# Kernel optimization log

Measured on AMD Instinct MI355X. Metric: run time of the kernel, lower is better.

The kernel has to match this reference:

```python
import jax, jax.numpy as jnp
import numpy as np

B, L, H, K = 4, 4096, 2048, 4
EPS = 1e-5

def setup_inputs() -> dict:
    key = jax.random.key(0)
    k1, k2, k3, k4 = jax.random.split(key, 4)
    x = jax.random.normal(k1, (B, L, H), dtype=jnp.float32)
    # depthwise Conv1d weight: (out_channels=H, in_channels/groups=1, K)
    w = jax.random.normal(k2, (H, 1, K), dtype=jnp.float32) * (1.0 / np.sqrt(K))
    gamma = jax.random.uniform(k3, (H,), dtype=jnp.float32, minval=0.5, maxval=1.5)
    beta = jax.random.normal(k4, (H,), dtype=jnp.float32) * 0.05
    return {"x": x, "w": w, "gamma": gamma, "beta": beta}

def reference(x, w, gamma, beta):
    # x: (B, L, H) -> (B, H, L) channels-first like torch Conv1d
    xc = jnp.transpose(x, (0, 2, 1))
    k = w.shape[-1]
    h = w.shape[0]
    # causal depthwise conv: left-pad K-1, groups = H
    y = jax.lax.conv_general_dilated(
        xc, w,
        window_strides=(1,),
        padding=[(k - 1, 0)],
        feature_group_count=h,
        dimension_numbers=("NCH", "OIH", "NCH"),
    )
    # residual: x_padded[:, :, K-1:] == original xc
    y = y + xc
    y = jnp.transpose(y, (0, 2, 1))  # (B, L, H)
    # LayerNorm over hidden dim
    mu = jnp.mean(y, axis=-1, keepdims=True)
    var = jnp.mean(jnp.square(y - mu), axis=-1, keepdims=True)
    out = (y - mu) * jax.lax.rsqrt(var + EPS) * gamma + beta
    return out
```

## Files before the change

kernel.cpp:

```cpp
#include <hip/hip_runtime.h>

constexpr int B = 4;
constexpr int L = 4096;
constexpr int H = 2048;
constexpr int KTAP = 4;
constexpr float EPS = 1e-5f;

constexpr int THREADS = 256;
constexpr int H4 = H / 4;
constexpr int COLS = H4 / THREADS;
constexpr int ROWS = 8;
constexpr int TILES = (B * L) / ROWS;
constexpr int TPB = L / ROWS;
constexpr int NXCD = 8;
constexpr int WAVES = THREADS / 64;

__global__ __launch_bounds__(THREADS)
void fused_conv_res_ln(const float4* __restrict__ x4,
                       const float4* __restrict__ w4,
                       const float4* __restrict__ g4,
                       const float4* __restrict__ bt4,
                       float4* __restrict__ o4)
{
    const int bid     = blockIdx.x;
    const int logical = (bid & (NXCD - 1)) * (TILES / NXCD) + (bid >> 3);
    const int b       = logical / TPB;
    const int tile    = logical - b * TPB;
    const int l0      = tile * ROWS;
    const int t       = threadIdx.x;

    const size_t rowbase = (size_t)b * L;

    float4 xw[COLS][KTAP];
    float4 wc[COLS][4];
    float4 gg[COLS], bb[COLS];
    int    jj[COLS];

    #pragma unroll
    for (int c = 0; c < COLS; ++c) {
        const int j = t + c * THREADS;
        jj[c] = j;
        #pragma unroll
        for (int k = 0; k < 4; ++k) wc[c][k] = w4[4 * j + k];
        gg[c] = g4[j];
        bb[c] = bt4[j];
        #pragma unroll
        for (int k = 0; k < 3; ++k) {
            const int lr = l0 - 3 + k;
            xw[c][k] = (lr >= 0) ? x4[(rowbase + lr) * H4 + j]
                                 : make_float4(0.f, 0.f, 0.f, 0.f);
        }
        xw[c][3] = x4[(rowbase + l0) * H4 + j];
    }

    __shared__ float s_sum[ROWS][WAVES];
    __shared__ float s_sq [ROWS][WAVES];
    const int wave = t >> 6;
    const int lane = t & 63;

    #pragma unroll
    for (int r = 0; r < ROWS; ++r) {
        float4 xn[COLS];
        if (r + 1 < ROWS) {
            #pragma unroll
            for (int c = 0; c < COLS; ++c)
                xn[c] = x4[(rowbase + l0 + r + 1) * H4 + jj[c]];
        }

        float y[COLS][4];
        float sum = 0.f, sq = 0.f;
        #pragma unroll
        for (int c = 0; c < COLS; ++c) {
            const float4 a0 = xw[c][0], a1 = xw[c][1], a2 = xw[c][2], a3 = xw[c][3];
            y[c][0] = a0.x * wc[c][0].x + a1.x * wc[c][0].y + a2.x * wc[c][0].z + a3.x * wc[c][0].w + a3.x;
            y[c][1] = a0.y * wc[c][1].x + a1.y * wc[c][1].y + a2.y * wc[c][1].z + a3.y * wc[c][1].w + a3.y;
            y[c][2] = a0.z * wc[c][2].x + a1.z * wc[c][2].y + a2.z * wc[c][2].z + a3.z * wc[c][2].w + a3.z;
            y[c][3] = a0.w * wc[c][3].x + a1.w * wc[c][3].y + a2.w * wc[c][3].z + a3.w * wc[c][3].w + a3.w;
            sum += y[c][0] + y[c][1] + y[c][2] + y[c][3];
            sq  += y[c][0] * y[c][0] + y[c][1] * y[c][1]
                 + y[c][2] * y[c][2] + y[c][3] * y[c][3];
        }

        #pragma unroll
        for (int off = 32; off > 0; off >>= 1) {
            sum += __shfl_down(sum, off, 64);
            sq  += __shfl_down(sq,  off, 64);
        }
        if (lane == 0) { s_sum[r][wave] = sum; s_sq[r][wave] = sq; }
        __syncthreads();

        float tot = 0.f, totq = 0.f;
        #pragma unroll
        for (int i = 0; i < WAVES; ++i) { tot += s_sum[r][i]; totq += s_sq[r][i]; }

        const float inv_h = 1.0f / (float)H;
        const float mu    = tot * inv_h;
        const float var   = totq * inv_h - mu * mu;
        const float rstd  = rsqrtf(var + EPS);

        #pragma unroll
        for (int c = 0; c < COLS; ++c) {
            float4 o;
            o.x = (y[c][0] - mu) * rstd * gg[c].x + bb[c].x;
            o.y = (y[c][1] - mu) * rstd * gg[c].y + bb[c].y;
            o.z = (y[c][2] - mu) * rstd * gg[c].z + bb[c].z;
            o.w = (y[c][3] - mu) * rstd * gg[c].w + bb[c].w;
            o4[(rowbase + l0 + r) * H4 + jj[c]] = o;
        }

        #pragma unroll
        for (int c = 0; c < COLS; ++c) {
            xw[c][0] = xw[c][1];
            xw[c][1] = xw[c][2];
            xw[c][2] = xw[c][3];
            if (r + 1 < ROWS) xw[c][3] = xn[c];
        }
    }
}

extern "C" void kernel_launch(void* const* d_in, const int* in_sizes, int n_in,
                              void* d_out, int out_size, void* d_ws, size_t ws_size,
                              hipStream_t stream) {
    const float4* x     = (const float4*)d_in[0];
    const float4* w     = (const float4*)d_in[1];
    const float4* gamma = (const float4*)d_in[2];
    const float4* beta  = (const float4*)d_in[3];
    float4* out = (float4*)d_out;

    dim3 grid(TILES);
    dim3 block(THREADS);
    fused_conv_res_ln<<<grid, block, 0, stream>>>(x, w, gamma, beta, out);
}
```

Baseline: 249.0 us.

## Map one wave per row and drop block-level LayerNorm reduction

Restructures the kernel so each 64-lane wave handles a whole hidden row (8 float4 per lane) instead of a 256-thread block sweeping an 8-row tile with a sliding register window. The row statistics now come from a wave-only xor-shuffle reduction, which removes the shared-memory stage and the per-row __syncthreads. The cost is that each row now re-reads its three predecessor rows from global memory (4x logical x reads, expected to hit cache) and reloads weights, gamma and beta per row. Launch bounds now request 4 blocks per CU to raise occupancy.

```diff
diff --git a/kernel.cpp b/kernel.cpp
--- a/kernel.cpp
+++ b/kernel.cpp
@@ -3,19 +3,17 @@
 constexpr int B = 4;
 constexpr int L = 4096;
 constexpr int H = 2048;
-constexpr int KTAP = 4;
 constexpr float EPS = 1e-5f;
 
+constexpr int H4 = H / 4;
 constexpr int THREADS = 256;
-constexpr int H4 = H / 4;
-constexpr int COLS = H4 / THREADS;
-constexpr int ROWS = 8;
-constexpr int TILES = (B * L) / ROWS;
-constexpr int TPB = L / ROWS;
+constexpr int WPB = THREADS / 64;
+constexpr int NROWS = B * L;
+constexpr int GRID = NROWS / WPB;
 constexpr int NXCD = 8;
-constexpr int WAVES = THREADS / 64;
+constexpr int CHUNK = GRID / NXCD;
 
-__global__ __launch_bounds__(THREADS)
+__global__ __launch_bounds__(THREADS, 4)
 void fused_conv_res_ln(const float4* __restrict__ x4,
                        const float4* __restrict__ w4,
                        const float4* __restrict__ g4,
@@ -23,98 +21,86 @@
                        float4* __restrict__ o4)
 {
     const int bid     = blockIdx.x;
-    const int logical = (bid & (NXCD - 1)) * (TILES / NXCD) + (bid >> 3);
-    const int b       = logical / TPB;
-    const int tile    = logical - b * TPB;
-    const int l0      = tile * ROWS;
-    const int t       = threadIdx.x;
+    const int logical = (bid & (NXCD - 1)) * CHUNK + (bid >> 3);
+    const int wave    = threadIdx.x >> 6;
+    const int lane    = threadIdx.x & 63;
 
-    const size_t rowbase = (size_t)b * L;
+    const int row = logical * WPB + wave;
+    const int l   = row & (L - 1);
 
-    float4 xw[COLS][KTAP];
-    float4 wc[COLS][4];
-    float4 gg[COLS], bb[COLS];
-    int    jj[COLS];
+    const float4* xr   = x4 + (size_t)row * H4;
+    float4*       orow = o4 + (size_t)row * H4;
+
+    float4 y[8];
+    float sum = 0.f, sq = 0.f;
+
+    if (l >= 3) {
+        #pragma unroll
+        for (int c = 0; c < 8; ++c) {
+            const int j = lane + (c << 6);
+            const float4 a0 = xr[j - 3 * H4];
+            const float4 a1 = xr[j - 2 * H4];
+            const float4 a2 = xr[j - 1 * H4];
+            const float4 a3 = xr[j];
+            const float4 w0 = w4[4 * j + 0];
+            const float4 w1 = w4[4 * j + 1];
+            const float4 w2 = w4[4 * j + 2];
+            const float4 w3 = w4[4 * j + 3];
+            float4 yy;
+            yy.x = a0.x * w0.x + a1.x * w0.y + a2.x * w0.z + a3.x * w0.w + a3.x;
+            yy.y = a0.y * w1.x + a1.y * w1.y + a2.y * w1.z + a3.y * w1.w + a3.y;
+            yy.z = a0.z * w2.x + a1.z * w2.y + a2.z * w2.z + a3.z * w2.w + a3.z;
+            yy.w = a0.w * w3.x + a1.w * w3.y + a2.w * w3.z + a3.w * w3.w + a3.w;
+            y[c] = yy;
+            sum += yy.x + yy.y + yy.z + yy.w;
+            sq  += yy.x * yy.x + yy.y * yy.y + yy.z * yy.z + yy.w * yy.w;
+        }
+    } else {
+        const float4 z = make_float4(0.f, 0.f, 0.f, 0.f);
+        #pragma unroll
+        for (int c = 0; c < 8; ++c) {
+            const int j = lane + (c << 6);
+            const float4 a0 = z;
+            const float4 a1 = (l >= 2) ? xr[j - 2 * H4] : z;
+            const float4 a2 = (l >= 1) ? xr[j - 1 * H4] : z;
+            const float4 a3 = xr[j];
+            const float4 w0 = w4[4 * j + 0];
+            const float4 w1 = w4[4 * j + 1];
+            const float4 w2 = w4[4 * j + 2];
+            const float4 w3 = w4[4 * j + 3];
+            float4 yy;
+            yy.x = a0.x * w0.x + a1.x * w0.y + a2.x * w0.z + a3.x * w0.w + a3.x;
+            yy.y = a0.y * w1.x + a1.y * w1.y + a2.y * w1.z + a3.y * w1.w + a3.y;
+            yy.z = a0.z * w2.x + a1.z * w2.y + a2.z * w2.z + a3.z * w2.w + a3.z;
+            yy.w = a0.w * w3.x + a1.w * w3.y + a2.w * w3.z + a3.w * w3.w + a3.w;
+            y[c] = yy;
+            sum += yy.x + yy.y + yy.z + yy.w;
+            sq  += yy.x * yy.x + yy.y * yy.y + yy.z * yy.z + yy.w * yy.w;
+        }
+    }
 
     #pragma unroll
-    for (int c = 0; c < COLS; ++c) {
-        const int j = t + c * THREADS;
-        jj[c] = j;
-        #pragma unroll
-        for (int k = 0; k < 4; ++k) wc[c][k] = w4[4 * j + k];
-        gg[c] = g4[j];
-        bb[c] = bt4[j];
-        #pragma unroll
-        for (int k = 0; k < 3; ++k) {
-            const int lr = l0 - 3 + k;
-            xw[c][k] = (lr >= 0) ? x4[(rowbase + lr) * H4 + j]
-                                 : make_float4(0.f, 0.f, 0.f, 0.f);
-        }
-        xw[c][3] = x4[(rowbase + l0) * H4 + j];
+    for (int off = 1; off < 64; off <<= 1) {
+        sum += __shfl_xor(sum, off, 64);
+        sq  += __shfl_xor(sq,  off, 64);
     }
 
-    __shared__ float s_sum[ROWS][WAVES];
-    __shared__ float s_sq [ROWS][WAVES];
-    const int wave = t >> 6;
-    const int lane = t & 63;
+    const float inv_h = 1.0f / (float)H;
+    const float mu    = sum * inv_h;
+    const float var   = sq * inv_h - mu * mu;
+    const float rstd  = rsqrtf(var + EPS);
 
     #pragma unroll
-    for (int r = 0; r < ROWS; ++r) {
-        float4 xn[COLS];
-        if (r + 1 < ROWS) {
-            #pragma unroll
-            for (int c = 0; c < COLS; ++c)
-                xn[c] = x4[(rowbase + l0 + r + 1) * H4 + jj[c]];
-        }
-
-        float y[COLS][4];
-        float sum = 0.f, sq = 0.f;
-        #pragma unroll
-        for (int c = 0; c < COLS; ++c) {
-            const float4 a0 = xw[c][0], a1 = xw[c][1], a2 = xw[c][2], a3 = xw[c][3];
-            y[c][0] = a0.x * wc[c][0].x + a1.x * wc[c][0].y + a2.x * wc[c][0].z + a3.x * wc[c][0].w + a3.x;
-            y[c][1] = a0.y * wc[c][1].x + a1.y * wc[c][1].y + a2.y * wc[c][1].z + a3.y * wc[c][1].w + a3.y;
-            y[c][2] = a0.z * wc[c][2].x + a1.z * wc[c][2].y + a2.z * wc[c][2].z + a3.z * wc[c][2].w + a3.z;
-            y[c][3] = a0.w * wc[c][3].x + a1.w * wc[c][3].y + a2.w * wc[c][3].z + a3.w * wc[c][3].w + a3.w;
-            sum += y[c][0] + y[c][1] + y[c][2] + y[c][3];
-            sq  += y[c][0] * y[c][0] + y[c][1] * y[c][1]
-                 + y[c][2] * y[c][2] + y[c][3] * y[c][3];
-        }
-
-        #pragma unroll
-        for (int off = 32; off > 0; off >>= 1) {
-            sum += __shfl_down(sum, off, 64);
-            sq  += __shfl_down(sq,  off, 64);
-        }
-        if (lane == 0) { s_sum[r][wave] = sum; s_sq[r][wave] = sq; }
-        __syncthreads();
-
-        float tot = 0.f, totq = 0.f;
-        #pragma unroll
-        for (int i = 0; i < WAVES; ++i) { tot += s_sum[r][i]; totq += s_sq[r][i]; }
-
-        const float inv_h = 1.0f / (float)H;
-        const float mu    = tot * inv_h;
-        const float var   = totq * inv_h - mu * mu;
-        const float rstd  = rsqrtf(var + EPS);
-
-        #pragma unroll
-        for (int c = 0; c < COLS; ++c) {
-            float4 o;
-            o.x = (y[c][0] - mu) * rstd * gg[c].x + bb[c].x;
-            o.y = (y[c][1] - mu) * rstd * gg[c].y + bb[c].y;
-            o.z = (y[c][2] - mu) * rstd * gg[c].z + bb[c].z;
-            o.w = (y[c][3] - mu) * rstd * gg[c].w + bb[c].w;
-            o4[(rowbase + l0 + r) * H4 + jj[c]] = o;
-        }
-
-        #pragma unroll
-        for (int c = 0; c < COLS; ++c) {
-            xw[c][0] = xw[c][1];
-            xw[c][1] = xw[c][2];
-            xw[c][2] = xw[c][3];
-            if (r + 1 < ROWS) xw[c][3] = xn[c];
-        }
+    for (int c = 0; c < 8; ++c) {
+        const int j = lane + (c << 6);
+        const float4 g  = g4[j];
+        const float4 be = bt4[j];
+        float4 o;
+        o.x = (y[c].x - mu) * rstd * g.x + be.x;
+        o.y = (y[c].y - mu) * rstd * g.y + be.y;
+        o.z = (y[c].z - mu) * rstd * g.z + be.z;
+        o.w = (y[c].w - mu) * rstd * g.w + be.w;
+        orow[j] = o;
     }
 }
 
@@ -127,7 +113,5 @@
     const float4* beta  = (const float4*)d_in[3];
     float4* out = (float4*)d_out;
 
-    dim3 grid(TILES);
-    dim3 block(THREADS);
-    fused_conv_res_ln<<<grid, block, 0, stream>>>(x, w, gamma, beta, out);
+    fused_conv_res_ln<<<dim3(GRID), dim3(THREADS), 0, stream>>>(x, w, gamma, beta, out);
 }
```

Measured after the change: 339.5 us. 1.36x slower.

## Batch LayerNorm reductions into a single barrier after computing all tile rows

Applied to the files above, without the earlier changes.

Instead of a __syncthreads per row, the kernel now computes the conv+residual for all 8 rows, keeps the results in registers (y[ROWS][COLS]), writes per-wave partial sums to shared memory, and does one barrier before normalizing and storing every row. Gamma/beta loads are deferred until after the barrier, the wave reduction uses xor shuffles, and launch bounds request 2 blocks per CU. This removes per-row barrier stalls and lets loads for later rows overlap with compute, at the cost of many more live registers (8x2 float4 outputs), which may spill or reduce occupancy.

```diff
diff --git a/kernel.cpp b/kernel.cpp
--- a/kernel.cpp
+++ b/kernel.cpp
@@ -3,11 +3,10 @@
 constexpr int B = 4;
 constexpr int L = 4096;
 constexpr int H = 2048;
-constexpr int KTAP = 4;
 constexpr float EPS = 1e-5f;
 
+constexpr int H4 = H / 4;
 constexpr int THREADS = 256;
-constexpr int H4 = H / 4;
 constexpr int COLS = H4 / THREADS;
 constexpr int ROWS = 8;
 constexpr int TILES = (B * L) / ROWS;
@@ -15,7 +14,7 @@
 constexpr int NXCD = 8;
 constexpr int WAVES = THREADS / 64;
 
-__global__ __launch_bounds__(THREADS)
+__global__ __launch_bounds__(THREADS, 2)
 void fused_conv_res_ln(const float4* __restrict__ x4,
                        const float4* __restrict__ w4,
                        const float4* __restrict__ g4,
@@ -28,35 +27,36 @@
     const int tile    = logical - b * TPB;
     const int l0      = tile * ROWS;
     const int t       = threadIdx.x;
+    const int wave    = t >> 6;
+    const int lane    = t & 63;
 
     const size_t rowbase = (size_t)b * L;
 
-    float4 xw[COLS][KTAP];
+    int    jj[COLS];
     float4 wc[COLS][4];
-    float4 gg[COLS], bb[COLS];
-    int    jj[COLS];
-
     #pragma unroll
     for (int c = 0; c < COLS; ++c) {
-        const int j = t + c * THREADS;
-        jj[c] = j;
+        jj[c] = t + c * THREADS;
         #pragma unroll
-        for (int k = 0; k < 4; ++k) wc[c][k] = w4[4 * j + k];
-        gg[c] = g4[j];
-        bb[c] = bt4[j];
+        for (int k = 0; k < 4; ++k) wc[c][k] = w4[4 * jj[c] + k];
+    }
+
+    float4 xw[COLS][4];
+    #pragma unroll
+    for (int c = 0; c < COLS; ++c) {
         #pragma unroll
         for (int k = 0; k < 3; ++k) {
             const int lr = l0 - 3 + k;
-            xw[c][k] = (lr >= 0) ? x4[(rowbase + lr) * H4 + j]
+            xw[c][k] = (lr >= 0) ? x4[(rowbase + lr) * H4 + jj[c]]
                                  : make_float4(0.f, 0.f, 0.f, 0.f);
         }
-        xw[c][3] = x4[(rowbase + l0) * H4 + j];
+        xw[c][3] = x4[(rowbase + l0) * H4 + jj[c]];
     }
 
     __shared__ float s_sum[ROWS][WAVES];
     __shared__ float s_sq [ROWS][WAVES];
-    const int wave = t >> 6;
-    const int lane = t & 63;
+
+    float4 y[ROWS][COLS];
 
     #pragma unroll
     for (int r = 0; r < ROWS; ++r) {
@@ -67,46 +67,26 @@
                 xn[c] = x4[(rowbase + l0 + r + 1) * H4 + jj[c]];
         }
 
-        float y[COLS][4];
         float sum = 0.f, sq = 0.f;
         #pragma unroll
         for (int c = 0; c < COLS; ++c) {
             const float4 a0 = xw[c][0], a1 = xw[c][1], a2 = xw[c][2], a3 = xw[c][3];
-            y[c][0] = a0.x * wc[c][0].x + a1.x * wc[c][0].y + a2.x * wc[c][0].z + a3.x * wc[c][0].w + a3.x;
-            y[c][1] = a0.y * wc[c][1].x + a1.y * wc[c][1].y + a2.y * wc[c][1].z + a3.y * wc[c][1].w + a3.y;
-            y[c][2] = a0.z * wc[c][2].x + a1.z * wc[c][2].y + a2.z * wc[c][2].z + a3.z * wc[c][2].w + a3.z;
-            y[c][3] = a0.w * wc[c][3].x + a1.w * wc[c][3].y + a2.w * wc[c][3].z + a3.w * wc[c][3].w + a3.w;
-            sum += y[c][0] + y[c][1] + y[c][2] + y[c][3];
-            sq  += y[c][0] * y[c][0] + y[c][1] * y[c][1]
-                 + y[c][2] * y[c][2] + y[c][3] * y[c][3];
+            float4 yy;
+            yy.x = a0.x * wc[c][0].x + a1.x * wc[c][0].y + a2.x * wc[c][0].z + a3.x * wc[c][0].w + a3.x;
+            yy.y = a0.y * wc[c][1].x + a1.y * wc[c][1].y + a2.y * wc[c][1].z + a3.y * wc[c][1].w + a3.y;
+            yy.z = a0.z * wc[c][2].x + a1.z * wc[c][2].y + a2.z * wc[c][2].z + a3.z * wc[c][2].w + a3.z;
+            yy.w = a0.w * wc[c][3].x + a1.w * wc[c][3].y + a2.w * wc[c][3].z + a3.w * wc[c][3].w + a3.w;
+            y[r][c] = yy;
+            sum += yy.x + yy.y + yy.z + yy.w;
+            sq  += yy.x * yy.x + yy.y * yy.y + yy.z * yy.z + yy.w * yy.w;
         }
 
         #pragma unroll
-        for (int off = 32; off > 0; off >>= 1) {
-            sum += __shfl_down(sum, off, 64);
-            sq  += __shfl_down(sq,  off, 64);
+        for (int off = 1; off < 64; off <<= 1) {
+            sum += __shfl_xor(sum, off, 64);
+            sq  += __shfl_xor(sq,  off, 64);
         }
         if (lane == 0) { s_sum[r][wave] = sum; s_sq[r][wave] = sq; }
-        __syncthreads();
-
-        float tot = 0.f, totq = 0.f;
-        #pragma unroll
-        for (int i = 0; i < WAVES; ++i) { tot += s_sum[r][i]; totq += s_sq[r][i]; }
-
-        const float inv_h = 1.0f / (float)H;
-        const float mu    = tot * inv_h;
-        const float var   = totq * inv_h - mu * mu;
-        const float rstd  = rsqrtf(var + EPS);
-
-        #pragma unroll
-        for (int c = 0; c < COLS; ++c) {
-            float4 o;
-            o.x = (y[c][0] - mu) * rstd * gg[c].x + bb[c].x;
-            o.y = (y[c][1] - mu) * rstd * gg[c].y + bb[c].y;
-            o.z = (y[c][2] - mu) * rstd * gg[c].z + bb[c].z;
-            o.w = (y[c][3] - mu) * rstd * gg[c].w + bb[c].w;
-            o4[(rowbase + l0 + r) * H4 + jj[c]] = o;
-        }
 
         #pragma unroll
         for (int c = 0; c < COLS; ++c) {
@@ -114,6 +94,33 @@
             xw[c][1] = xw[c][2];
             xw[c][2] = xw[c][3];
             if (r + 1 < ROWS) xw[c][3] = xn[c];
+        }
+    }
+
+    __syncthreads();
+
+    float4 gg[COLS], bb[COLS];
+    #pragma unroll
+    for (int c = 0; c < COLS; ++c) { gg[c] = g4[jj[c]]; bb[c] = bt4[jj[c]]; }
+
+    const float inv_h = 1.0f / (float)H;
+    #pragma unroll
+    for (int r = 0; r < ROWS; ++r) {
+        float tot = 0.f, totq = 0.f;
+        #pragma unroll
+        for (int i = 0; i < WAVES; ++i) { tot += s_sum[r][i]; totq += s_sq[r][i]; }
+        const float mu   = tot * inv_h;
+        const float var  = totq * inv_h - mu * mu;
+        const float rstd = rsqrtf(var + EPS);
+
+        #pragma unroll
+        for (int c = 0; c < COLS; ++c) {
+            float4 o;
+            o.x = (y[r][c].x - mu) * rstd * gg[c].x + bb[c].x;
+            o.y = (y[r][c].y - mu) * rstd * gg[c].y + bb[c].y;
+            o.z = (y[r][c].z - mu) * rstd * gg[c].z + bb[c].z;
+            o.w = (y[r][c].w - mu) * rstd * gg[c].w + bb[c].w;
+            o4[(rowbase + l0 + r) * H4 + jj[c]] = o;
         }
     }
 }
@@ -127,7 +134,5 @@
     const float4* beta  = (const float4*)d_in[3];
     float4* out = (float4*)d_out;
 
-    dim3 grid(TILES);
-    dim3 block(THREADS);
-    fused_conv_res_ln<<<grid, block, 0, stream>>>(x, w, gamma, beta, out);
+    fused_conv_res_ln<<<dim3(TILES), dim3(THREADS), 0, stream>>>(x, w, gamma, beta, out);
 }
```

New measurement: 247.5 us. Within noise of the previous version (-0.6%).
